# Optimization experiments

Hardware: AMD Instinct MI355X
Metric: run time of the kernel (lower is better)

The kernel has to match this reference:

```python
import jax, jax.numpy as jnp
import numpy as np

T, B, U = 512, 64, 64
H, N, C, L, IN = 400, 10, 20, 60, 3
SCALE = 0.05  # attention_scale


def setup_inputs() -> dict:
    key = jax.random.key(0)
    ks = jax.random.split(key, 16)
    s = 0.05  # ~1/sqrt(H) init scale
    r = lambda k, shape, sc: jax.random.normal(k, shape, jnp.float32) * sc
    return {
        "strokes_inputs": r(ks[0], (T, B, IN), 1.0),
        "text_inputs": jax.random.randint(ks[1], (B, U), 0, L),
        "text_lengths": jax.random.randint(ks[2], (B,), 1, U + 1),
        "h0_h": jnp.zeros((B, H)), "h0_c": jnp.zeros((B, H)),
        "h1_h": jnp.zeros((B, H)), "h1_c": jnp.zeros((B, H)),
        "h2_h": jnp.zeros((B, H)), "h2_c": jnp.zeros((B, H)),
        "prev_w_t": jnp.zeros((B, L)), "prev_k": jnp.zeros((B, N)),
        "W_ih0": r(ks[3], (4 * H, IN + L), s), "W_hh0": r(ks[4], (4 * H, H), s),
        "b_ih0": jnp.zeros((4 * H,)), "b_hh0": jnp.zeros((4 * H,)),
        "W_ih1": r(ks[5], (4 * H, H + IN + L), s), "W_hh1": r(ks[6], (4 * H, H), s),
        "b_ih1": jnp.zeros((4 * H,)), "b_hh1": jnp.zeros((4 * H,)),
        "W_ih2": r(ks[7], (4 * H, H + IN + L), s), "W_hh2": r(ks[8], (4 * H, H), s),
        "b_ih2": jnp.zeros((4 * H,)), "b_hh2": jnp.zeros((4 * H,)),
        "W_win": r(ks[9], (3 * N, H), s), "b_win": jnp.zeros((3 * N,)),
        "W_mu": r(ks[10], (2 * C, 3 * H), s), "b_mu": jnp.zeros((2 * C,)),
        "W_ls": r(ks[11], (2 * C, 3 * H), s), "b_ls": jnp.zeros((2 * C,)),
        "W_rho": r(ks[12], (C, 3 * H), s), "b_rho": jnp.zeros((C,)),
        "W_pi": r(ks[13], (C, 3 * H), s), "b_pi": jnp.zeros((C,)),
        "W_eos": r(ks[14], (1, 3 * H), s), "b_eos": jnp.zeros((1,)),
    }


def _lstm_cell(x, h, c, Wih, Whh, bih, bhh):
    # torch nn.LSTM gate order: input, forget, cell(g), output
    g = x @ Wih.T + bih + h @ Whh.T + bhh
    i, f, gg, o = jnp.split(g, 4, axis=-1)
    c = jax.nn.sigmoid(f) * c + jax.nn.sigmoid(i) * jnp.tanh(gg)
    h = jax.nn.sigmoid(o) * jnp.tanh(c)
    return h, c


def reference(strokes_inputs, text_inputs, text_lengths, h0_h, h0_c, h1_h, h1_c, h2_h, h2_c,
              prev_w_t, prev_k, W_ih0, W_hh0, b_ih0, b_hh0, W_ih1, W_hh1, b_ih1, b_hh1,
              W_ih2, W_hh2, b_ih2, b_hh2, W_win, b_win, W_mu, b_mu, W_ls, b_ls,
              W_rho, b_rho, W_pi, b_pi, W_eos, b_eos):
    onehot = jax.nn.one_hot(text_inputs, L, dtype=jnp.float32)   # [B,U,L]
    u_idx = jnp.arange(U, dtype=jnp.float32)                      # [U]
    mask = (jnp.arange(U)[None, :] < text_lengths[:, None]).astype(jnp.float32)  # [B,U]

    # layer 0 + Graves Gaussian-window attention (sequential via k recurrence)
    def step0(carry, x):
        h, c, w, k = carry
        h, c = _lstm_cell(jnp.concatenate([x, w], -1), h, c, W_ih0, W_hh0, b_ih0, b_hh0)
        o = h @ W_win.T + b_win                                   # [B,3N]
        a = jnp.exp(o[:, :N])
        b = jnp.exp(o[:, N:2 * N])
        k = jnp.exp(o[:, 2 * N:]) * SCALE + k                     # [B,N]
        phi = jnp.sum(a[:, :, None] * jnp.exp(-b[:, :, None] * (k[:, :, None] - u_idx) ** 2), axis=1) * mask  # [B,U]
        w = jnp.einsum('bu,bul->bl', phi, onehot)                 # [B,L]
        return (h, c, w, k), (h, w, phi)

    (h0_h, h0_c, prev_w_t, prev_k), (y0, w_ts, alignments) = jax.lax.scan(
        step0, (h0_h, h0_c, prev_w_t, prev_k), strokes_inputs)

    def mk_step(Wih, Whh, bih, bhh):
        def step(carry, x):
            h, c = _lstm_cell(x, carry[0], carry[1], Wih, Whh, bih, bhh)
            return (h, c), h
        return step

    rnn1_in = jnp.concatenate([y0, w_ts, strokes_inputs], -1)     # [T,B,H+L+3]
    (h1_h, h1_c), y1 = jax.lax.scan(mk_step(W_ih1, W_hh1, b_ih1, b_hh1), (h1_h, h1_c), rnn1_in)
    rnn2_in = jnp.concatenate([y1, w_ts, strokes_inputs], -1)
    (h2_h, h2_c), y2 = jax.lax.scan(mk_step(W_ih2, W_hh2, b_ih2, b_hh2), (h2_h, h2_c), rnn2_in)

    rnn_out = jnp.concatenate([y0, y1, y2], -1)                   # [T,B,3H]
    means = (rnn_out @ W_mu.T + b_mu).reshape(T, B, C, 2)
    log_sigmas = (rnn_out @ W_ls.T + b_ls).reshape(T, B, C, 2)
    correlations = jnp.tanh(rnn_out @ W_rho.T + b_rho)            # [T,B,C]
    pi_logits = rnn_out @ W_pi.T + b_pi                           # [T,B,C]
    eos_logits = rnn_out @ W_eos.T + b_eos                        # [T,B,1]
    return (means, log_sigmas, correlations, pi_logits, eos_logits,
            h0_h, h0_c, h1_h, h1_c, h2_h, h2_c, prev_w_t, prev_k, alignments)
```

## Files before the change

### kernel.cpp

```cpp
#include <hip/hip_runtime.h>

typedef unsigned short u16;
typedef __attribute__((ext_vector_type(8))) short short8;
typedef __attribute__((ext_vector_type(4))) float float4v;

#define NT 512

#define O_MEANS 0
#define O_LS    1310720
#define O_RHO   2621440
#define O_PI    3276800
#define O_EOS   3932160
#define O_H0H   3964928
#define O_H0C   3990528
#define O_H1H   4016128
#define O_H1C   4041728
#define O_H2H   4067328
#define O_H2C   4092928
#define O_PW    4118528
#define O_PK    4122368
#define O_AL    4123008

#define GBASE(g)  (256 + (g)*1024)
#define FGOFF     832
#define SPIN_MAX  (1L<<19)

struct P {
  const float *strokes; const int *text; const int *tlen;
  const float *h0h,*h0c,*h1h,*h1c,*h2h,*h2c,*pw,*pk;
  const float *bih0,*bhh0,*bih1,*bhh1,*bih2,*bhh2;
  const float *Wwin,*bwin;
  const float *bmu,*bls,*brho,*bpi,*beos;
  u16 *B0,*B1,*B2,*Bw0,*BP;
  u16 *A0,*A1,*A2;
  u16 *y0,*y1,*y2;
  float *obuf;
  unsigned *bar;
  float *out;
};

__device__ __forceinline__ u16 f2bf(float f){
  unsigned int x = __float_as_uint(f);
  unsigned int r = x + 0x7FFFu + ((x >> 16) & 1u);
  return (u16)(r >> 16);
}
__device__ __forceinline__ size_t aidx(int t, int b, int k, int KB){
  return ((size_t)((t*4 + (b>>4))*KB + (k>>5)))*512
       + (size_t)(((((k>>3)&3)*16) + (b&15))*8 + (k&7));
}
__device__ __forceinline__ float sigm(float x){ return 1.f/(1.f+__expf(-x)); }
__device__ __forceinline__ float tanh_f(float x){ return 2.f/(1.f+__expf(-2.f*x)) - 1.f; }

__global__ void kpackB(const float* __restrict__ Wih, const float* __restrict__ Whh,
                       u16* __restrict__ dst, int KB, int kx, int stride, int total){
  int tid = blockIdx.x*256 + threadIdx.x;
  if (tid >= total) return;
  int e = tid & 511, blk = tid >> 9;
  int kb = blk % KB, tile = (blk / KB) & 3, s = blk / (KB*4);
  int lane = e >> 3, j = e & 7;
  int q = lane >> 4, n = lane & 15;
  int k = kb*32 + q*8 + j;
  int col = s*16 + tile*4 + (n&3);
  int g = (n>>2)*400 + col;
  float v = 0.f;
  if (k < kx) v = Wih[(size_t)g*stride + k];
  else if (k < kx + 400) v = Whh[(size_t)g*400 + (k - kx)];
  dst[tid] = f2bf(v);
}

__global__ void kpackBw(const float* __restrict__ Wih0, u16* __restrict__ dst){
  int tid = blockIdx.x*256 + threadIdx.x;
  if (tid >= 25*4*2*512) return;
  int e = tid & 511, blk = tid >> 9;
  int kb = blk & 1, tile = (blk>>1) & 3, s = blk >> 3;
  int lane = e >> 3, j = e & 7;
  int q = lane >> 4, n = lane & 15;
  int k = kb*32 + q*8 + j;
  int col = s*16 + tile*4 + (n&3);
  int g = (n>>2)*400 + col;
  dst[tid] = (k < 60) ? f2bf(Wih0[(size_t)g*63 + 3 + k]) : (u16)0;
}

__global__ void kpackBP(const float* __restrict__ Wmu, const float* __restrict__ Wls,
                        const float* __restrict__ Wrho, const float* __restrict__ Wpi,
                        const float* __restrict__ Weos, u16* __restrict__ dst){
  int tid = blockIdx.x*256 + threadIdx.x;
  if (tid >= 8*38*512) return;
  int e = tid & 511, blk = tid >> 9;
  int lane = e >> 3, j = e & 7;
  int ns = blk / 38, kb = blk % 38;
  int q = lane >> 4, n = lane & 15;
  int k = kb*32 + q*8 + j;
  int col = ns*16 + n;
  float v = 0.f;
  if (k < 1200){
    if (col < 40)       v = Wmu[(size_t)col*1200 + k];
    else if (col < 80)  v = Wls[(size_t)(col-40)*1200 + k];
    else if (col < 100) v = Wrho[(size_t)(col-80)*1200 + k];
    else if (col < 120) v = Wpi[(size_t)(col-100)*1200 + k];
    else if (col == 120) v = Weos[k];
  }
  dst[tid] = f2bf(v);
}

__global__ void kfillA(P p){
  int tid = blockIdx.x*256 + threadIdx.x;
  if (tid >= 512*64*32) return;
  int it = tid & 31; int rr = tid >> 5; int b = rr & 63; int t = rr >> 6;
  const float* sx = p.strokes + ((size_t)t*64 + b)*3;
  if (it < 3)        p.A0[aidx(t,b,it,13)] = f2bf(sx[it]);
  else if (it < 16)  p.A0[aidx(t,b,400+it,13)] = 0;
  else if (it < 19)  p.A1[aidx(t,b,460+(it-16),27)] = f2bf(sx[it-16]);
  else if (it == 19) p.A1[aidx(t,b,863,27)] = 0;
  else if (it < 23)  p.A2[aidx(t,b,460+(it-20),27)] = f2bf(sx[it-20]);
  else if (it == 23) p.A2[aidx(t,b,863,27)] = 0;
}

__global__ void kinit(P p){
  int tid = blockIdx.x*256 + threadIdx.x;
  if (tid < 25600){ int b=tid/400, j=tid%400; p.A0[aidx(0,b,3+j,13)] = f2bf(p.h0h[tid]); }
  else if (tid < 51200){ int i=tid-25600; int b=i/400, j=i%400; p.A1[aidx(0,b,463+j,27)] = f2bf(p.h1h[i]); }
  else if (tid < 76800){ int i=tid-51200; int b=i/400, j=i%400; p.A2[aidx(0,b,463+j,27)] = f2bf(p.h2h[i]); }
  else if (tid < 105600){ p.obuf[tid-76800] = 0.f; }
  else if (tid < 109696){ p.bar[tid-105600] = 0u; }
}

__device__ __forceinline__ void gsyncx(unsigned* fl, int s, unsigned target){
  __threadfence_block();
  __syncthreads();
  if (threadIdx.x == 0)
    __hip_atomic_store(&fl[s*32], target, __ATOMIC_RELAXED, __HIP_MEMORY_SCOPE_AGENT);
  if (threadIdx.x < 25){
    long c = 0;
    while (__hip_atomic_load(&fl[threadIdx.x*32], __ATOMIC_RELAXED, __HIP_MEMORY_SCOPE_AGENT) < target){
      __builtin_amdgcn_s_sleep(1);
      if (++c > SPIN_MAX) break;
    }
  }
  __syncthreads();
}

__device__ __forceinline__ void waitgen(const unsigned* gw, unsigned target){
  if (threadIdx.x == 0){
    long c = 0;
    while (__hip_atomic_load(gw, __ATOMIC_RELAXED, __HIP_MEMORY_SCOPE_AGENT) < target){
      __builtin_amdgcn_s_sleep(1);
      if (++c > SPIN_MAX) break;
    }
  }
  __syncthreads();
}

__global__ __launch_bounds__(NT, 1) void kmain(P p){
  const int tid = threadIdx.x;
  const int lane = tid & 63, wave = tid >> 6;
  const int bq = wave & 3, th = wave >> 2;

  __shared__ int role2[2];
  if (tid == 0){
    unsigned x;
    asm volatile("s_getreg_b32 %0, hwreg(HW_REG_XCC_ID, 0, 4)" : "=s"(x));
    x &= 7u;
    unsigned sl = atomicAdd(&p.bar[x*32], 1u);
    role2[0] = (int)x; role2[1] = (int)sl;
  }
  __syncthreads();
  const int grp = role2[0];
  const int s   = role2[1];
  if (grp > 2 || s > 25) return;
  unsigned* fl = p.bar + GBASE(grp);

  if (s == 25){
    if (grp == 2) return;
    if (tid < 25){
      unsigned* fg = fl + FGOFF;
      for (unsigned rr = 1; rr <= 514; ++rr){
        long c = 0;
        while (__hip_atomic_load(&fl[tid*32], __ATOMIC_RELAXED, __HIP_MEMORY_SCOPE_AGENT) < rr){
          __builtin_amdgcn_s_sleep(2);
          if (++c > SPIN_MAX) break;
        }
        if (tid == 0){
          __builtin_amdgcn_fence(__ATOMIC_RELEASE, "agent");
          __hip_atomic_store(fg, rr, __ATOMIC_RELAXED, __HIP_MEMORY_SCOPE_AGENT);
        }
      }
    }
    return;
  }

  const int lag = (grp == 0) ? 0 : (grp + 1);

  __shared__ u16  wB[55296];
  __shared__ float ldsg[64][65];
  __shared__ float clds[16][64];
  __shared__ float bsum[64];

  u16* wBw = wB + 26624;
  char* exb = (char*)(wB + 30720);
  float (*hsh)[64]  = (float (*)[64])(exb);
  float (*wacc)[64] = (float (*)[64])(exb + 4096);
  u16   (*wbf)[80]  = (u16   (*)[80])(exb + 19456);
  float (*klds)[10] = (float (*)[10])(exb + 29696);
  float (*ash)[10]  = (float (*)[10])(exb + 32256);
  float (*bsh)[10]  = (float (*)[10])(exb + 34816);
  float (*ksh)[10]  = (float (*)[10])(exb + 37376);
  float (*wwin_l)[16] = (float (*)[16])(exb + 39936);
  unsigned char* text_l = (unsigned char*)(exb + 41856);
  int*   tlen_l = (int*)(exb + 45952);
  float* bwin_l = (float*)(exb + 46208);

  const u16 *Ap; u16 *yr;
  const float *bi, *bh, *cin; int ohh, occ;
  if (grp == 0){ Ap=p.A0; yr=p.y0; bi=p.bih0; bh=p.bhh0; cin=p.h0c; ohh=O_H0H; occ=O_H0C; }
  else if (grp == 1){ Ap=p.A1; yr=p.y1; bi=p.bih1; bh=p.bhh1; cin=p.h1c; ohh=O_H1H; occ=O_H1C; }
  else { Ap=p.A2; yr=p.y2; bi=p.bih2; bh=p.bhh2; cin=p.h2c; ohh=O_H2H; occ=O_H2C; }

  {
    const u16* gsrc; int cnt;
    if (grp == 0){ gsrc = p.B0 + (size_t)s*26624; cnt = 26624; }
    else if (grp == 1){ gsrc = p.B1 + (size_t)s*55296; cnt = 55296; }
    else { gsrc = p.B2 + (size_t)s*55296; cnt = 55296; }
    for (int i = tid*8; i < cnt; i += NT*8)
      *reinterpret_cast<short8*>(&wB[i]) = *reinterpret_cast<const short8*>(gsrc + i);
    if (grp == 0){
      const u16* gw = p.Bw0 + (size_t)s*4096;
      for (int i = tid*8; i < 4096; i += NT*8)
        *reinterpret_cast<short8*>(wBw + i) = *reinterpret_cast<const short8*>(gw + i);
    }
  }

  for (int cell = tid; cell < 1024; cell += NT){
    int jj = cell >> 6, b = cell & 63;
    clds[jj][b] = cin[b*400 + s*16 + jj];
  }
  if (tid < 64){
    int jj = tid >> 2, gg = tid & 3;
    bsum[tid] = bi[gg*400 + s*16 + jj] + bh[gg*400 + s*16 + jj];
  }
  if (grp == 0){
    for (int cell = tid; cell < 640; cell += NT) klds[cell/10][cell%10] = p.pk[cell];
    for (int cell = tid; cell < 64*80; cell += NT){
      int b = cell/80, k = cell%80;
      wbf[b][k] = (k < 60) ? f2bf(p.pw[b*60 + k]) : (u16)0;
    }
    for (int cell = tid; cell < 480; cell += NT)
      wwin_l[cell>>4][cell&15] = p.Wwin[(cell>>4)*400 + s*16 + (cell&15)];
    for (int cell = tid; cell < 4096; cell += NT)
      text_l[cell] = (unsigned char)p.text[cell];
    if (tid < 64) tlen_l[tid] = p.tlen[tid];
    if (tid < 30) bwin_l[tid] = p.bwin[tid];
  }
  __syncthreads();

  for (int r = 0; r < 515; ++r){
    const int t = r - lag;

    if (grp == 1 && r >= 2 && r <= 513) waitgen(p.bar + GBASE(0) + FGOFF, (unsigned)r);
    if (grp == 2 && r >= 3 && r <= 514) waitgen(p.bar + GBASE(1) + FGOFF, (unsigned)r);

    float ovs[4][5];
    if (grp == 0 && r >= 1 && r <= 512){
      const float* ob = p.obuf + (size_t)((r-1)%3)*9600;
      #pragma unroll
      for (int i = 0; i < 4; ++i){
        int cell = tid + i*NT;
        if (cell < 1920){
          #pragma unroll
          for (int bk = 0; bk < 5; ++bk)
            ovs[i][bk] = __hip_atomic_load(&ob[bk*1920 + cell], __ATOMIC_RELAXED, __HIP_MEMORY_SCOPE_AGENT);
        }
      }
    }
    short8 a0r[13];
    if (grp == 0 && t < 512){
      const u16* Ab = p.A0 + ((size_t)(t*4 + bq)*13)*512 + (size_t)lane*8;
      #pragma unroll
      for (int kb = 0; kb < 13; ++kb)
        a0r[kb] = *reinterpret_cast<const short8*>(Ab + (size_t)kb*512);
    }

    if (grp == 0 && r >= 1 && r <= 512){
      const int tw = r - 1;
      #pragma unroll
      for (int i = 0; i < 4; ++i){
        int cell = tid + i*NT;
        if (cell < 1920){
          int b = cell & 63, n = cell >> 6;
          float o = ovs[i][0]+ovs[i][1]+ovs[i][2]+ovs[i][3]+ovs[i][4] + bwin_l[n];
          if (n < 10) ash[b][n] = __expf(o);
          else if (n < 20) bsh[b][n-10] = __expf(o);
          else { float kn = klds[b][n-20] + 0.05f*__expf(o); klds[b][n-20] = kn; ksh[b][n-20] = kn; }
        }
      }
      for (int cell = tid; cell < 3840; cell += NT) ((float*)wacc)[cell] = 0.f;
      __syncthreads();
      for (int cell = tid; cell < 4096; cell += NT){
        int b = cell >> 6, u = cell & 63;
        float phi = 0.f;
        if (u < tlen_l[b]){
          #pragma unroll
          for (int n = 0; n < 10; ++n){
            float d = ksh[b][n] - (float)u;
            phi += ash[b][n]*__expf(-bsh[b][n]*d*d);
          }
          atomicAdd(&wacc[text_l[b*64 + u]][b], phi);
        }
        if (((cell*25) >> 12) == s)
          p.out[O_AL + ((size_t)tw*64 + b)*64 + u] = phi;
      }
      __syncthreads();
      for (int cell = tid; cell < 3840; cell += NT){
        int b = cell & 63, l = cell >> 6;
        u16 wv = f2bf(wacc[l][b]);
        wbf[b][l] = wv;
        if (s == 1) p.A1[aidx(tw,b,400+l,27)] = wv;
        if (s == 2) p.A2[aidx(tw,b,400+l,27)] = wv;
        if (s == 0 && tw == 511) p.out[O_PW + b*60 + l] = wacc[l][b];
      }
      if (s == 0 && tw == 511)
        for (int cell = tid; cell < 640; cell += NT) p.out[O_PK + cell] = klds[cell/10][cell%10];
      __syncthreads();
    }

    if (t >= 0 && t < 512){
      float4v acc[2] = {{0.f,0.f,0.f,0.f},{0.f,0.f,0.f,0.f}};
      if (grp == 0){
        #pragma unroll
        for (int kb = 0; kb < 13; ++kb){
          #pragma unroll
          for (int u2 = 0; u2 < 2; ++u2){
            int tt = th*2 + u2;
            short8 bf = *reinterpret_cast<const short8*>(wB + (size_t)(tt*13 + kb)*512 + (size_t)lane*8);
            acc[u2] = __builtin_amdgcn_mfma_f32_16x16x32_bf16(a0r[kb], bf, acc[u2], 0, 0, 0);
          }
        }
        const int m = lane & 15, q = (lane >> 4) & 3;
        #pragma unroll
        for (int kb = 0; kb < 2; ++kb){
          short8 af = *reinterpret_cast<const short8*>(&wbf[bq*16 + m][kb*32 + q*8]);
          #pragma unroll
          for (int u2 = 0; u2 < 2; ++u2){
            int tt = th*2 + u2;
            short8 bf = *reinterpret_cast<const short8*>(wBw + (size_t)((tt*2 + kb))*512 + (size_t)lane*8);
            acc[u2] = __builtin_amdgcn_mfma_f32_16x16x32_bf16(af, bf, acc[u2], 0, 0, 0);
          }
        }
      } else {
        short8 a1r[27];
        const u16* Ab = Ap + ((size_t)(t*4 + bq)*27)*512 + (size_t)lane*8;
        #pragma unroll
        for (int kb = 0; kb < 27; ++kb)
          a1r[kb] = *reinterpret_cast<const short8*>(Ab + (size_t)kb*512);
        #pragma unroll
        for (int kb = 0; kb < 27; ++kb){
          #pragma unroll
          for (int u2 = 0; u2 < 2; ++u2){
            int tt = th*2 + u2;
            short8 bf = *reinterpret_cast<const short8*>(wB + (size_t)(tt*27 + kb)*512 + (size_t)lane*8);
            acc[u2] = __builtin_amdgcn_mfma_f32_16x16x32_bf16(a1r[kb], bf, acc[u2], 0, 0, 0);
          }
        }
      }
      {
        const int c = lane & 15, rb = bq*16 + ((lane>>4)<<2);
        #pragma unroll
        for (int u2 = 0; u2 < 2; ++u2){
          int tt = th*2 + u2;
          #pragma unroll
          for (int rr2 = 0; rr2 < 4; ++rr2)
            ldsg[rb+rr2][tt*16 + c] = acc[u2][rr2];
        }
      }
      __syncthreads();
      for (int cell = tid; cell < 1024; cell += NT){
        int jj = cell >> 6, b = cell & 63;
        int j = s*16 + jj, tt = jj >> 2, jo = jj & 3;
        float gi = ldsg[b][tt*16 +      jo] + bsum[jj*4 + 0];
        float gf = ldsg[b][tt*16 +  4 + jo] + bsum[jj*4 + 1];
        float gg = ldsg[b][tt*16 +  8 + jo] + bsum[jj*4 + 2];
        float go = ldsg[b][tt*16 + 12 + jo] + bsum[jj*4 + 3];
        float cp = clds[jj][b];
        float cn = sigm(gf)*cp + sigm(gi)*tanh_f(gg);
        float hh = sigm(go)*tanh_f(cn);
        clds[jj][b] = cn;
        u16 hb = f2bf(hh);
        yr[((size_t)t*64 + b)*400 + j] = hb;
        if (grp == 0){
          p.A1[aidx(t,b,j,27)] = hb;
          if (t < 511) p.A0[aidx(t+1,b,3+j,13)] = hb;
          hsh[jj][b] = hh;
        } else if (grp == 1){
          p.A2[aidx(t,b,j,27)] = hb;
          if (t < 511) p.A1[aidx(t+1,b,463+j,27)] = hb;
        } else {
          if (t < 511) p.A2[aidx(t+1,b,463+j,27)] = hb;
        }
        if (t == 511){ p.out[ohh + b*400 + j] = hh; p.out[occ + b*400 + j] = cn; }
      }
      if (grp == 0){
        __syncthreads();
        float* od = p.obuf + (size_t)(r%3)*9600 + (size_t)(s%5)*1920;
        for (int cell = tid; cell < 1920; cell += NT){
          int b = cell & 63, n = cell >> 6;
          float sum = 0.f;
          #pragma unroll
          for (int jj = 0; jj < 16; ++jj)
            sum += hsh[jj][b] * wwin_l[n][jj];
          atomicAdd(&od[n*64 + b], sum);
        }
      }
    }
    if (grp == 0 && r <= 510){
      float* oz = p.obuf + (size_t)((r+1)%3)*9600 + (size_t)s*384;
      for (int cell = tid; cell < 384; cell += NT)
        __hip_atomic_store(&oz[cell], 0.f, __ATOMIC_RELAXED, __HIP_MEMORY_SCOPE_AGENT);
    }
    if (r < 514) gsyncx(fl, s, (unsigned)(r+1));
  }
}

__global__ __launch_bounds__(256) void kproj(P p){
  const int t = blockIdx.x >> 3, ns = blockIdx.x & 7;
  const int tid = threadIdx.x, lane = tid & 63, wave = tid >> 6;
  const int m = lane & 15, q = lane >> 4;
  float4v acc = {0.f,0.f,0.f,0.f};
  const size_t rowA = (size_t)t*64 + wave*16 + m;
  const u16* Bb = p.BP + ((size_t)ns*38)*512 + (size_t)lane*8;
  for (int kb = 0; kb < 38; ++kb){
    int k0 = kb*32 + q*8;
    const u16* src; int off;
    if (k0 < 400){ src = p.y0; off = k0; }
    else if (k0 < 800){ src = p.y1; off = k0 - 400; }
    else if (k0 < 1200){ src = p.y2; off = k0 - 800; }
    else { src = p.y0; off = 0; }
    short8 af = *reinterpret_cast<const short8*>(src + rowA*400 + off);
    short8 bf = *reinterpret_cast<const short8*>(Bb + (size_t)kb*512);
    acc = __builtin_amdgcn_mfma_f32_16x16x32_bf16(af, bf, acc, 0, 0, 0);
  }
  const int j = ns*16 + (lane & 15);
  const int bo = wave*16 + q*4;
  #pragma unroll
  for (int rr = 0; rr < 4; ++rr){
    float v = acc[rr];
    size_t ro = (size_t)t*64 + bo + rr;
    if (j < 40)        p.out[O_MEANS + ro*40 + j]        = v + p.bmu[j];
    else if (j < 80)   p.out[O_LS    + ro*40 + (j-40)]   = v + p.bls[j-40];
    else if (j < 100)  p.out[O_RHO   + ro*20 + (j-80)]   = tanhf(v + p.brho[j-80]);
    else if (j < 120)  p.out[O_PI    + ro*20 + (j-100)]  = v + p.bpi[j-100];
    else if (j == 120) p.out[O_EOS   + ro]               = v + p.beos[0];
  }
}

extern "C" void kernel_launch(void* const* d_in, const int* in_sizes, int n_in,
                              void* d_out, int out_size, void* d_ws, size_t ws_size,
                              hipStream_t stream){
  P p;
  p.strokes = (const float*)d_in[0];
  p.text    = (const int*)  d_in[1];
  p.tlen    = (const int*)  d_in[2];
  p.h0h = (const float*)d_in[3];  p.h0c = (const float*)d_in[4];
  p.h1h = (const float*)d_in[5];  p.h1c = (const float*)d_in[6];
  p.h2h = (const float*)d_in[7];  p.h2c = (const float*)d_in[8];
  p.pw  = (const float*)d_in[9];  p.pk  = (const float*)d_in[10];
  const float* Wih0 = (const float*)d_in[11]; const float* Whh0 = (const float*)d_in[12];
  p.bih0 = (const float*)d_in[13]; p.bhh0 = (const float*)d_in[14];
  const float* Wih1 = (const float*)d_in[15]; const float* Whh1 = (const float*)d_in[16];
  p.bih1 = (const float*)d_in[17]; p.bhh1 = (const float*)d_in[18];
  const float* Wih2 = (const float*)d_in[19]; const float* Whh2 = (const float*)d_in[20];
  p.bih2 = (const float*)d_in[21]; p.bhh2 = (const float*)d_in[22];
  p.Wwin = (const float*)d_in[23]; p.bwin = (const float*)d_in[24];
  const float* Wmu  = (const float*)d_in[25]; p.bmu  = (const float*)d_in[26];
  const float* Wls  = (const float*)d_in[27]; p.bls  = (const float*)d_in[28];
  const float* Wrho = (const float*)d_in[29]; p.brho = (const float*)d_in[30];
  const float* Wpi  = (const float*)d_in[31]; p.bpi  = (const float*)d_in[32];
  const float* Weos = (const float*)d_in[33]; p.beos = (const float*)d_in[34];
  p.out = (float*)d_out;

  char* w = (char*)d_ws; size_t off = 0;
  auto alloc = [&](size_t bytes)->void*{ void* r = w + off; off += (bytes + 511) & ~(size_t)511; return r; };
  p.B0  = (u16*)alloc((size_t)25*4*13*512*2);
  p.B1  = (u16*)alloc((size_t)25*4*27*512*2);
  p.B2  = (u16*)alloc((size_t)25*4*27*512*2);
  p.Bw0 = (u16*)alloc((size_t)25*4*2*512*2);
  p.BP  = (u16*)alloc((size_t)8*38*512*2);
  p.A0  = (u16*)alloc((size_t)512*4*13*512*2);
  p.A1  = (u16*)alloc((size_t)512*4*27*512*2);
  p.A2  = (u16*)alloc((size_t)512*4*27*512*2);
  p.y0  = (u16*)alloc((size_t)512*64*400*2);
  p.y1  = (u16*)alloc((size_t)512*64*400*2);
  p.y2  = (u16*)alloc((size_t)512*64*400*2);
  p.obuf= (float*)alloc((size_t)3*9600*4);
  p.bar = (unsigned*)alloc((size_t)4096*4);

  kpackB<<<dim3(2600), dim3(256), 0, stream>>>(Wih0, Whh0, p.B0, 13, 3,   63,  25*4*13*512);
  kpackB<<<dim3(5400), dim3(256), 0, stream>>>(Wih1, Whh1, p.B1, 27, 463, 463, 25*4*27*512);
  kpackB<<<dim3(5400), dim3(256), 0, stream>>>(Wih2, Whh2, p.B2, 27, 463, 463, 25*4*27*512);
  kpackBw<<<dim3(400), dim3(256), 0, stream>>>(Wih0, p.Bw0);
  kpackBP<<<dim3(608), dim3(256), 0, stream>>>(Wmu, Wls, Wrho, Wpi, Weos, p.BP);
  kfillA<<<dim3(4096), dim3(256), 0, stream>>>(p);
  kinit<<<dim3(429), dim3(256), 0, stream>>>(p);

  kmain<<<dim3(256), dim3(NT), 0, stream>>>(p);

  kproj<<<dim3(4096), dim3(256), 0, stream>>>(p);
}
```

Measured before the change: 6.599 ms.

## Double block threads so each wave computes one gate tile in the recurrent step

Raises the persistent recurrent kernel's block size from 512 to 1024 threads, so each wave owns a single 16-column MFMA tile instead of two. The strided element loops become single guarded assignments, and the attention-window phi loop is restructured so each thread handles four positions with the window parameters held in registers. The layer-1/2 A-operand loads are split into three chunks of nine to limit register pressure. This shortens the serial per-step critical path through more parallelism, at the cost of more wave scheduling, tighter per-thread register limits under 1024-thread launch bounds and possibly higher barrier cost.

```diff
diff --git a/kernel.cpp b/kernel.cpp
--- a/kernel.cpp
+++ b/kernel.cpp
@@ -4,7 +4,7 @@
 typedef __attribute__((ext_vector_type(8))) short short8;
 typedef __attribute__((ext_vector_type(4))) float float4v;
 
-#define NT 512
+#define NT 1024
 
 #define O_MEANS 0
 #define O_LS    1310720
@@ -225,13 +225,13 @@
       *reinterpret_cast<short8*>(&wB[i]) = *reinterpret_cast<const short8*>(gsrc + i);
     if (grp == 0){
       const u16* gw = p.Bw0 + (size_t)s*4096;
-      for (int i = tid*8; i < 4096; i += NT*8)
-        *reinterpret_cast<short8*>(wBw + i) = *reinterpret_cast<const short8*>(gw + i);
-    }
-  }
-
-  for (int cell = tid; cell < 1024; cell += NT){
-    int jj = cell >> 6, b = cell & 63;
+      if (tid*8 < 4096)
+        *reinterpret_cast<short8*>(wBw + tid*8) = *reinterpret_cast<const short8*>(gw + tid*8);
+    }
+  }
+
+  if (tid < 1024){
+    int jj = tid >> 6, b = tid & 63;
     clds[jj][b] = cin[b*400 + s*16 + jj];
   }
   if (tid < 64){
@@ -239,13 +239,12 @@
     bsum[tid] = bi[gg*400 + s*16 + jj] + bh[gg*400 + s*16 + jj];
   }
   if (grp == 0){
-    for (int cell = tid; cell < 640; cell += NT) klds[cell/10][cell%10] = p.pk[cell];
+    if (tid < 640) klds[tid/10][tid%10] = p.pk[tid];
     for (int cell = tid; cell < 64*80; cell += NT){
       int b = cell/80, k = cell%80;
       wbf[b][k] = (k < 60) ? f2bf(p.pw[b*60 + k]) : (u16)0;
     }
-    for (int cell = tid; cell < 480; cell += NT)
-      wwin_l[cell>>4][cell&15] = p.Wwin[(cell>>4)*400 + s*16 + (cell&15)];
+    if (tid < 480) wwin_l[tid>>4][tid&15] = p.Wwin[(tid>>4)*400 + s*16 + (tid&15)];
     for (int cell = tid; cell < 4096; cell += NT)
       text_l[cell] = (unsigned char)p.text[cell];
     if (tid < 64) tlen_l[tid] = p.tlen[tid];
@@ -259,11 +258,11 @@
     if (grp == 1 && r >= 2 && r <= 513) waitgen(p.bar + GBASE(0) + FGOFF, (unsigned)r);
     if (grp == 2 && r >= 3 && r <= 514) waitgen(p.bar + GBASE(1) + FGOFF, (unsigned)r);
 
-    float ovs[4][5];
+    float ovs[2][5];
     if (grp == 0 && r >= 1 && r <= 512){
       const float* ob = p.obuf + (size_t)((r-1)%3)*9600;
       #pragma unroll
-      for (int i = 0; i < 4; ++i){
+      for (int i = 0; i < 2; ++i){
         int cell = tid + i*NT;
         if (cell < 1920){
           #pragma unroll
@@ -283,7 +282,7 @@
     if (grp == 0 && r >= 1 && r <= 512){
       const int tw = r - 1;
       #pragma unroll
-      for (int i = 0; i < 4; ++i){
+      for (int i = 0; i < 2; ++i){
         int cell = tid + i*NT;
         if (cell < 1920){
           int b = cell & 63, n = cell >> 6;
@@ -295,19 +294,35 @@
       }
       for (int cell = tid; cell < 3840; cell += NT) ((float*)wacc)[cell] = 0.f;
       __syncthreads();
-      for (int cell = tid; cell < 4096; cell += NT){
-        int b = cell >> 6, u = cell & 63;
-        float phi = 0.f;
-        if (u < tlen_l[b]){
+      {
+        const int b = tid >> 4, u0 = (tid & 15) * 4;
+        const int tl = tlen_l[b];
+        float ph[4] = {0.f, 0.f, 0.f, 0.f};
+        if (u0 < tl){
+          float av[10], bv[10], kv[10];
           #pragma unroll
-          for (int n = 0; n < 10; ++n){
-            float d = ksh[b][n] - (float)u;
-            phi += ash[b][n]*__expf(-bsh[b][n]*d*d);
+          for (int n = 0; n < 10; ++n){ av[n]=ash[b][n]; bv[n]=bsh[b][n]; kv[n]=ksh[b][n]; }
+          #pragma unroll
+          for (int j = 0; j < 4; ++j){
+            int u = u0 + j;
+            if (u < tl){
+              float phi = 0.f;
+              #pragma unroll
+              for (int n = 0; n < 10; ++n){
+                float d = kv[n] - (float)u;
+                phi += av[n]*__expf(-bv[n]*d*d);
+              }
+              ph[j] = phi;
+              atomicAdd(&wacc[text_l[b*64 + u]][b], phi);
+            }
           }
-          atomicAdd(&wacc[text_l[b*64 + u]][b], phi);
-        }
-        if (((cell*25) >> 12) == s)
-          p.out[O_AL + ((size_t)tw*64 + b)*64 + u] = phi;
+        }
+        #pragma unroll
+        for (int j = 0; j < 4; ++j){
+          int cell = tid*4 + j;
+          if (((cell*25) >> 12) == s)
+            p.out[O_AL + ((size_t)tw*64 + b)*64 + u0 + j] = ph[j];
+        }
       }
       __syncthreads();
       for (int cell = tid; cell < 3840; cell += NT){
@@ -318,63 +333,49 @@
         if (s == 2) p.A2[aidx(tw,b,400+l,27)] = wv;
         if (s == 0 && tw == 511) p.out[O_PW + b*60 + l] = wacc[l][b];
       }
-      if (s == 0 && tw == 511)
-        for (int cell = tid; cell < 640; cell += NT) p.out[O_PK + cell] = klds[cell/10][cell%10];
+      if (s == 0 && tw == 511 && tid < 640) p.out[O_PK + tid] = klds[tid/10][tid%10];
       __syncthreads();
     }
 
     if (t >= 0 && t < 512){
-      float4v acc[2] = {{0.f,0.f,0.f,0.f},{0.f,0.f,0.f,0.f}};
+      float4v acc = {0.f,0.f,0.f,0.f};
       if (grp == 0){
         #pragma unroll
         for (int kb = 0; kb < 13; ++kb){
-          #pragma unroll
-          for (int u2 = 0; u2 < 2; ++u2){
-            int tt = th*2 + u2;
-            short8 bf = *reinterpret_cast<const short8*>(wB + (size_t)(tt*13 + kb)*512 + (size_t)lane*8);
-            acc[u2] = __builtin_amdgcn_mfma_f32_16x16x32_bf16(a0r[kb], bf, acc[u2], 0, 0, 0);
-          }
+          short8 bf = *reinterpret_cast<const short8*>(wB + (size_t)(th*13 + kb)*512 + (size_t)lane*8);
+          acc = __builtin_amdgcn_mfma_f32_16x16x32_bf16(a0r[kb], bf, acc, 0, 0, 0);
         }
         const int m = lane & 15, q = (lane >> 4) & 3;
         #pragma unroll
         for (int kb = 0; kb < 2; ++kb){
           short8 af = *reinterpret_cast<const short8*>(&wbf[bq*16 + m][kb*32 + q*8]);
-          #pragma unroll
-          for (int u2 = 0; u2 < 2; ++u2){
-            int tt = th*2 + u2;
-            short8 bf = *reinterpret_cast<const short8*>(wBw + (size_t)((tt*2 + kb))*512 + (size_t)lane*8);
-            acc[u2] = __builtin_amdgcn_mfma_f32_16x16x32_bf16(af, bf, acc[u2], 0, 0, 0);
-          }
+          short8 bf = *reinterpret_cast<const short8*>(wBw + (size_t)((th*2 + kb))*512 + (size_t)lane*8);
+          acc = __builtin_amdgcn_mfma_f32_16x16x32_bf16(af, bf, acc, 0, 0, 0);
         }
       } else {
-        short8 a1r[27];
         const u16* Ab = Ap + ((size_t)(t*4 + bq)*27)*512 + (size_t)lane*8;
         #pragma unroll
-        for (int kb = 0; kb < 27; ++kb)
-          a1r[kb] = *reinterpret_cast<const short8*>(Ab + (size_t)kb*512);
-        #pragma unroll
-        for (int kb = 0; kb < 27; ++kb){
+        for (int ch = 0; ch < 3; ++ch){
+          short8 a1r[9];
           #pragma unroll
-          for (int u2 = 0; u2 < 2; ++u2){
-            int tt = th*2 + u2;
-            short8 bf = *reinterpret_cast<const short8*>(wB + (size_t)(tt*27 + kb)*512 + (size_t)lane*8);
-            acc[u2] = __builtin_amdgcn_mfma_f32_16x16x32_bf16(a1r[kb], bf, acc[u2], 0, 0, 0);
+          for (int kb = 0; kb < 9; ++kb)
+            a1r[kb] = *reinterpret_cast<const short8*>(Ab + (size_t)(ch*9 + kb)*512);
+          #pragma unroll
+          for (int kb = 0; kb < 9; ++kb){
+            short8 bf = *reinterpret_cast<const short8*>(wB + (size_t)(th*27 + ch*9 + kb)*512 + (size_t)lane*8);
+            acc = __builtin_amdgcn_mfma_f32_16x16x32_bf16(a1r[kb], bf, acc, 0, 0, 0);
           }
         }
       }
       {
         const int c = lane & 15, rb = bq*16 + ((lane>>4)<<2);
         #pragma unroll
-        for (int u2 = 0; u2 < 2; ++u2){
-          int tt = th*2 + u2;
-          #pragma unroll
-          for (int rr2 = 0; rr2 < 4; ++rr2)
-            ldsg[rb+rr2][tt*16 + c] = acc[u2][rr2];
-        }
+        for (int rr2 = 0; rr2 < 4; ++rr2)
+          ldsg[rb+rr2][th*16 + c] = acc[rr2];
       }
       __syncthreads();
-      for (int cell = tid; cell < 1024; cell += NT){
-        int jj = cell >> 6, b = cell & 63;
+      if (tid < 1024){
+        int jj = tid >> 6, b = tid & 63;
         int j = s*16 + jj, tt = jj >> 2, jo = jj & 3;
         float gi = ldsg[b][tt*16 +      jo] + bsum[jj*4 + 0];
         float gf = ldsg[b][tt*16 +  4 + jo] + bsum[jj*4 + 1];
@@ -401,20 +402,23 @@
       if (grp == 0){
         __syncthreads();
         float* od = p.obuf + (size_t)(r%3)*9600 + (size_t)(s%5)*1920;
-        for (int cell = tid; cell < 1920; cell += NT){
-          int b = cell & 63, n = cell >> 6;
-          float sum = 0.f;
-          #pragma unroll
-          for (int jj = 0; jj < 16; ++jj)
-            sum += hsh[jj][b] * wwin_l[n][jj];
-          atomicAdd(&od[n*64 + b], sum);
-        }
-      }
-    }
-    if (grp == 0 && r <= 510){
+        #pragma unroll
+        for (int i = 0; i < 2; ++i){
+          int cell = tid + i*NT;
+          if (cell < 1920){
+            int b = cell & 63, n = cell >> 6;
+            float sum = 0.f;
+            #pragma unroll
+            for (int jj = 0; jj < 16; ++jj)
+              sum += hsh[jj][b] * wwin_l[n][jj];
+            atomicAdd(&od[n*64 + b], sum);
+          }
+        }
+      }
+    }
+    if (grp == 0 && r <= 510 && tid < 384){
       float* oz = p.obuf + (size_t)((r+1)%3)*9600 + (size_t)s*384;
-      for (int cell = tid; cell < 384; cell += NT)
-        __hip_atomic_store(&oz[cell], 0.f, __ATOMIC_RELAXED, __HIP_MEMORY_SCOPE_AGENT);
+      __hip_atomic_store(&oz[tid], 0.f, __ATOMIC_RELAXED, __HIP_MEMORY_SCOPE_AGENT);
     }
     if (r < 514) gsyncx(fl, s, (unsigned)(r+1));
   }
```

Result: slower. 9.875 ms (+49.6%).
